# Optimization experiments

Measured on AMD Instinct MI355X. Metric: run time of the kernel, lower is better.

The kernel has to match this reference:

```python
import jax, jax.numpy as jnp
import numpy as np

NUM_CLASSES = 1024
TAU = 1.0


def setup_inputs() -> dict:
    key = jax.random.key(0)
    k1, k2, k3 = jax.random.split(key, 3)
    N_s, N_q, D = 65536, 65536, 512
    z_support = jax.random.normal(k1, (N_s, D), dtype=jnp.float32)
    y_support = jax.random.randint(k2, (N_s,), 0, NUM_CLASSES, dtype=jnp.int64)
    z_query = jax.random.normal(k3, (N_q, D), dtype=jnp.float32)
    return {"z_support": z_support, "y_support": y_support, "z_query": z_query}


def reference(z_support, y_support, z_query):
    # Per-class mean prototypes via a single segment reduce.
    # (Assumes all classes 0..C-1 appear in y_support, so torch.unique remap is identity.)
    sums = jax.ops.segment_sum(z_support, y_support, num_segments=NUM_CLASSES)  # [C, D]
    counts = jax.ops.segment_sum(
        jnp.ones((z_support.shape[0],), dtype=z_support.dtype),
        y_support, num_segments=NUM_CLASSES)  # [C]
    protos = sums / jnp.maximum(counts, 1.0)[:, None]  # [C, D]

    # Pairwise squared euclidean: ||q||^2 + ||p||^2 - 2 q.p
    q_sq = jnp.sum(z_query * z_query, axis=-1, keepdims=True)          # [Nq, 1]
    p_sq = jnp.sum(protos * protos, axis=-1)[None, :]                  # [1, C]
    cross = jnp.einsum("nd,cd->nc", z_query, protos)                   # [Nq, C]
    dist = q_sq + p_sq - 2.0 * cross
    logits = -TAU * dist
    return logits
```

## Files before the change

kernel.cpp:

```cpp
#include <hip/hip_runtime.h>
#include <stdint.h>

#define C_CLASSES 1024
#define D_DIM     512
#define N_SUP     65536
#define N_QRY     65536
#define SLOTS     144

typedef float f32x4 __attribute__((ext_vector_type(4)));
typedef float f32x16v __attribute__((ext_vector_type(16)));
typedef short bf16x8 __attribute__((ext_vector_type(8)));
typedef unsigned short u16x4 __attribute__((ext_vector_type(4)));
typedef unsigned short u16x8 __attribute__((ext_vector_type(8)));

#define GLOBAL_AS __attribute__((address_space(1)))
#define LDS_AS    __attribute__((address_space(3)))

__device__ inline void async_copy16(const void* g, void* l) {
    __builtin_amdgcn_global_load_lds((const GLOBAL_AS void*)g, (LDS_AS void*)l, 16, 0, 0);
}

__device__ inline unsigned short f2bf(float f) {
    union { float f; unsigned int u; } x; x.f = f;
    unsigned int u = x.u;
    return (unsigned short)((u + 0x7fffu + ((u >> 16) & 1u)) >> 16);
}

__global__ void init_kernel(int* __restrict__ cursors) {
    cursors[threadIdx.x] = 0;
}

template<bool CONV>
__global__ __launch_bounds__(256) void qsq_conv_kernel(
    const float* __restrict__ zq, float* __restrict__ qsq,
    unsigned short* __restrict__ Abf,
    const int* __restrict__ ys, int* __restrict__ cursors,
    int* __restrict__ rowlist)
{
    if (blockIdx.x < N_SUP / 256) {
        int i = blockIdx.x * 256 + threadIdx.x;
        int c = ys[i];
        int slot = atomicAdd(&cursors[c], 1);
        if (slot < SLOTS) rowlist[c * SLOTS + slot] = i;
    }

    const int w    = threadIdx.x >> 6;
    const int lane = threadIdx.x & 63;
    const int row  = blockIdx.x * 4 + w;
    const f32x4* zp = (const f32x4*)(zq + (size_t)row * D_DIM);
    f32x4 a = zp[2 * lane];
    f32x4 b = zp[2 * lane + 1];
    if (CONV) {
        u16x8 p;
        p.s0 = f2bf(a.x); p.s1 = f2bf(a.y); p.s2 = f2bf(a.z); p.s3 = f2bf(a.w);
        p.s4 = f2bf(b.x); p.s5 = f2bf(b.y); p.s6 = f2bf(b.z); p.s7 = f2bf(b.w);
        *(u16x8*)(Abf + (size_t)row * D_DIM + lane * 8) = p;
    }
    float s = a.x*a.x + a.y*a.y + a.z*a.z + a.w*a.w
            + b.x*b.x + b.y*b.y + b.z*b.z + b.w*b.w;
    #pragma unroll
    for (int off = 32; off > 0; off >>= 1) s += __shfl_down(s, off, 64);
    if (lane == 0) qsq[row] = s;
}

__global__ __launch_bounds__(256) void proto_gather(
    const float* __restrict__ zs, const int* __restrict__ rowlist,
    const int* __restrict__ cursors, unsigned short* __restrict__ protos,
    float* __restrict__ psq)
{
    const int c    = blockIdx.x;
    const int tid  = threadIdx.x;
    const int w    = tid >> 6;
    const int lane = tid & 63;

    const int cnt = cursors[c];
    const int m   = cnt < SLOTS ? cnt : SLOTS;

    __shared__ int sRows[SLOTS];
    if (tid < m) sRows[tid] = rowlist[c * SLOTS + tid];
    __syncthreads();

    f32x4 s0 = {0.f, 0.f, 0.f, 0.f};
    f32x4 s1 = {0.f, 0.f, 0.f, 0.f};
    int j = w;
    for (; j + 4 < m; j += 8) {
        int r0 = sRows[j];
        int r1 = sRows[j + 4];
        const f32x4* z0 = (const f32x4*)(zs + (size_t)r0 * D_DIM);
        const f32x4* z1 = (const f32x4*)(zs + (size_t)r1 * D_DIM);
        f32x4 a0 = z0[lane], a1 = z0[64 + lane];
        f32x4 b0 = z1[lane], b1 = z1[64 + lane];
        s0 += a0; s1 += a1;
        s0 += b0; s1 += b1;
    }
    for (; j < m; j += 4) {
        int r = sRows[j];
        const f32x4* zp = (const f32x4*)(zs + (size_t)r * D_DIM);
        s0 += zp[lane];
        s1 += zp[64 + lane];
    }

    __shared__ float sAcc[4][D_DIM];
    ((f32x4*)&sAcc[w][0])[lane]      = s0;
    ((f32x4*)&sAcc[w][0])[64 + lane] = s1;
    __syncthreads();

    float inv = 1.0f / fmaxf((float)cnt, 1.0f);
    int t2 = tid + 256;
    float p0 = (sAcc[0][tid] + sAcc[1][tid] + sAcc[2][tid] + sAcc[3][tid]) * inv;
    float p1 = (sAcc[0][t2]  + sAcc[1][t2]  + sAcc[2][t2]  + sAcc[3][t2])  * inv;
    protos[(size_t)c * D_DIM + tid] = f2bf(p0);
    protos[(size_t)c * D_DIM + t2]  = f2bf(p1);

    float ps = p0 * p0 + p1 * p1;
    #pragma unroll
    for (int off = 32; off > 0; off >>= 1) ps += __shfl_down(ps, off, 64);
    __shared__ float sPs[4];
    if (lane == 0) sPs[w] = ps;
    __syncthreads();
    if (tid == 0) psq[c] = sPs[0] + sPs[1] + sPs[2] + sPs[3];
}

template<bool FAST>
__global__ __launch_bounds__(256) void gemm_kernel(
    const float* __restrict__ A32, const unsigned short* __restrict__ Abf,
    const unsigned short* __restrict__ Bp,
    const float* __restrict__ qsq, const float* __restrict__ psq,
    float* __restrict__ out)
{
    constexpr int BM = 128, BN = 128, BK = 64, K = D_DIM, NN = C_CLASSES;
    __shared__ __align__(16) unsigned short shA[BM * BK];
    __shared__ __align__(16) unsigned short shB[BN * BK];

    const int tid  = threadIdx.x;
    const int lane = tid & 63;
    const int w    = tid >> 6;
    const int wm   = w >> 1, wn = w & 1;
    const int l31  = lane & 31, half = lane >> 5;
    const int mBase = blockIdx.y * BM;
    const int nBase = blockIdx.x * BN;

    const int srow = lane >> 3;
    const int scg  = ((lane & 7) ^ srow) * 8;

    f32x16v acc[2][2];
    #pragma unroll
    for (int i = 0; i < 2; i++)
        #pragma unroll
        for (int j = 0; j < 2; j++)
            acc[i][j] = (f32x16v)(0.0f);

    for (int k0 = 0; k0 < K; k0 += BK) {
        __syncthreads();
        if (FAST) {
            #pragma unroll
            for (int t = 0; t < 4; t++) {
                int g = w * 4 + t;
                async_copy16(Abf + (size_t)(mBase + g * 8 + srow) * K + k0 + scg,
                             &shA[g * 8 * BK]);
                async_copy16(Bp  + (size_t)(nBase + g * 8 + srow) * K + k0 + scg,
                             &shB[g * 8 * BK]);
            }
        } else {
            #pragma unroll
            for (int t = 0; t < 4; t++) {
                int q = tid * 4 + t;
                int r = q >> 3;
                int x = q & 7;
                int cg = x ^ (r & 7);
                const float* src = A32 + (size_t)(mBase + r) * K + k0 + cg * 8;
                f32x4 v0 = *(const f32x4*)src;
                f32x4 v1 = *(const f32x4*)(src + 4);
                u16x8 p;
                p.s0 = f2bf(v0.x); p.s1 = f2bf(v0.y); p.s2 = f2bf(v0.z); p.s3 = f2bf(v0.w);
                p.s4 = f2bf(v1.x); p.s5 = f2bf(v1.y); p.s6 = f2bf(v1.z); p.s7 = f2bf(v1.w);
                *(u16x8*)&shA[r * BK + x * 8] = p;
            }
            #pragma unroll
            for (int t = 0; t < 4; t++) {
                int g = w * 4 + t;
                async_copy16(Bp + (size_t)(nBase + g * 8 + srow) * K + k0 + scg,
                             &shB[g * 8 * BK]);
            }
        }
        __syncthreads();

        bf16x8 af[2][4], bfv[2][4];
        #pragma unroll
        for (int i = 0; i < 2; i++) {
            int ra = wm * 64 + i * 32 + l31;
            int ga = ra & 7;
            int rb = wn * 64 + i * 32 + l31;
            int gb = rb & 7;
            #pragma unroll
            for (int ks = 0; ks < 4; ks++) {
                int c = ks * 2 + half;
                af[i][ks]  = *(const bf16x8*)&shA[ra * BK + ((c ^ ga) * 8)];
                bfv[i][ks] = *(const bf16x8*)&shB[rb * BK + ((c ^ gb) * 8)];
            }
        }
        #pragma unroll
        for (int ks = 0; ks < 4; ks++)
            #pragma unroll
            for (int i = 0; i < 2; i++)
                #pragma unroll
                for (int j = 0; j < 2; j++)
                    acc[i][j] = __builtin_amdgcn_mfma_f32_32x32x16_bf16(
                        af[i][ks], bfv[j][ks], acc[i][j], 0, 0, 0);
    }

    const int rowb = mBase + wm * 64;
    const int colb = nBase + wn * 64;
    float pv[2];
    #pragma unroll
    for (int j = 0; j < 2; j++) pv[j] = psq[colb + j * 32 + l31];
    #pragma unroll
    for (int i = 0; i < 2; i++) {
        #pragma unroll
        for (int rg = 0; rg < 4; rg++) {
            int rbase = rowb + i * 32 + rg * 8 + half * 4;
            f32x4 qv = *(const f32x4*)&qsq[rbase];
            #pragma unroll
            for (int rr = 0; rr < 4; rr++) {
                int reg = rg * 4 + rr;
                size_t rowoff = (size_t)(rbase + rr) * NN;
                #pragma unroll
                for (int j = 0; j < 2; j++) {
                    out[rowoff + colb + j * 32 + l31] =
                        2.0f * acc[i][j][reg] - qv[rr] - pv[j];
                }
            }
        }
    }
}

extern "C" void kernel_launch(void* const* d_in, const int* in_sizes, int n_in,
                              void* d_out, int out_size, void* d_ws, size_t ws_size,
                              hipStream_t stream) {
    const float* zs = (const float*)d_in[0];
    const int*   ys = (const int*)d_in[1];
    const float* zq = (const float*)d_in[2];
    float* out = (float*)d_out;

    const size_t szAbf     = (size_t)N_QRY * D_DIM * 2;
    const size_t szProtos  = (size_t)C_CLASSES * D_DIM * 2;
    const size_t szQsq     = (size_t)N_QRY * 4;
    const size_t szRowlist = (size_t)C_CLASSES * SLOTS * 4;
    const size_t szPsq     = 4096;
    const size_t szCur     = 4096;

    const size_t needFast = szAbf + szProtos + szQsq + szRowlist + szPsq + szCur;
    const bool fast = ws_size >= needFast;

    char* ws = (char*)d_ws;
    unsigned short* Abf = (unsigned short*)ws;
    char* base = fast ? ws + szAbf : ws;
    unsigned short* protos = (unsigned short*)base;
    float* qsq  = (float*)(base + szProtos);
    int*   rowlist = (int*)(base + szProtos + szQsq);
    float* psq  = (float*)(base + szProtos + szQsq + szRowlist);
    int*   cursors = (int*)(base + szProtos + szQsq + szRowlist + szPsq);

    init_kernel<<<1, C_CLASSES, 0, stream>>>(cursors);
    if (fast)
        qsq_conv_kernel<true><<<N_QRY / 4, 256, 0, stream>>>(
            zq, qsq, Abf, ys, cursors, rowlist);
    else
        qsq_conv_kernel<false><<<N_QRY / 4, 256, 0, stream>>>(
            zq, qsq, nullptr, ys, cursors, rowlist);
    proto_gather<<<C_CLASSES, 256, 0, stream>>>(zs, rowlist, cursors, protos, psq);
    if (fast)
        gemm_kernel<true><<<dim3(C_CLASSES / 128, N_QRY / 128), 256, 0, stream>>>(
            nullptr, Abf, protos, qsq, psq, out);
    else
        gemm_kernel<false><<<dim3(C_CLASSES / 128, N_QRY / 128), 256, 0, stream>>>(
            zq, nullptr, protos, qsq, psq, out);
}
```

Before: 544.8 us.

## Use 256x256 double-buffered GEMM tiles with interleaved async staging

Replaces the fast-path 128x128 GEMM with a 256x256 tile kernel using 512 threads and double-buffered LDS. It issues async global-to-LDS loads for the next K slice while running MFMAs on the current one, and raises wave priority around the MFMA block. It also swaps the cursor-zeroing kernel for a memset. The larger tiles and double buffering use 128KB of LDS and more accumulator registers, which lowers occupancy and leaves fewer blocks to fill the grid.

```diff
diff --git a/kernel.cpp b/kernel.cpp
--- a/kernel.cpp
+++ b/kernel.cpp
@@ -24,10 +24,6 @@
     union { float f; unsigned int u; } x; x.f = f;
     unsigned int u = x.u;
     return (unsigned short)((u + 0x7fffu + ((u >> 16) & 1u)) >> 16);
-}
-
-__global__ void init_kernel(int* __restrict__ cursors) {
-    cursors[threadIdx.x] = 0;
 }
 
 template<bool CONV>
@@ -121,9 +117,142 @@
     if (tid == 0) psq[c] = sPs[0] + sPs[1] + sPs[2] + sPs[3];
 }
 
-template<bool FAST>
-__global__ __launch_bounds__(256) void gemm_kernel(
-    const float* __restrict__ A32, const unsigned short* __restrict__ Abf,
+__device__ __forceinline__ void stage_half(
+    const unsigned short* __restrict__ src,
+    unsigned short* dstTile,
+    int rowBase,
+    size_t gBase,
+    int k0, int srow, int scg)
+{
+    async_copy16(src + (gBase + (size_t)(rowBase + srow)) * D_DIM + k0 + scg,
+                 dstTile + (size_t)rowBase * 64);
+}
+
+__global__ __launch_bounds__(512, 2) void gemm256_kernel(
+    const unsigned short* __restrict__ Abf,
+    const unsigned short* __restrict__ Bp,
+    const float* __restrict__ qsq, const float* __restrict__ psq,
+    float* __restrict__ out)
+{
+    constexpr int BM = 256, BN = 256, BK = 64, K = D_DIM, NN = C_CLASSES;
+    constexpr int NKT = K / BK;
+    __shared__ __align__(16) unsigned short shA[2][BM * BK];
+    __shared__ __align__(16) unsigned short shB[2][BN * BK];
+
+    const int tid  = threadIdx.x;
+    const int lane = tid & 63;
+    const int w    = tid >> 6;
+    const int wm   = w >> 2, wn = w & 3;
+    const int l31  = lane & 31, half = lane >> 5;
+    const int mBase = blockIdx.y * BM;
+    const int nBase = blockIdx.x * BN;
+
+    const int srow = lane >> 3;
+    const int scg  = ((lane & 7) ^ srow) * 8;
+
+    f32x16v acc[4][2];
+    #pragma unroll
+    for (int i = 0; i < 4; i++)
+        #pragma unroll
+        for (int j = 0; j < 2; j++)
+            acc[i][j] = (f32x16v)(0.0f);
+
+    #pragma unroll
+    for (int t = 0; t < 2; t++) {
+        int rb = (w * 2 + t) * 8;
+        stage_half(Abf, &shA[0][0], rb,       mBase, 0, srow, scg);
+        stage_half(Abf, &shA[0][0], 128 + rb, mBase, 0, srow, scg);
+        stage_half(Bp,  &shB[0][0], rb,       nBase, 0, srow, scg);
+        stage_half(Bp,  &shB[0][0], 128 + rb, nBase, 0, srow, scg);
+    }
+    asm volatile("s_waitcnt vmcnt(0)" ::: "memory");
+    __builtin_amdgcn_s_barrier();
+
+    for (int kt = 0; kt < NKT; ++kt) {
+        const int kn = kt + 1;
+        unsigned short* curA = &shA[kt & 1][0];
+        unsigned short* curB = &shB[kt & 1][0];
+        unsigned short* nxtA = &shA[kn & 1][0];
+        unsigned short* nxtB = &shB[kn & 1][0];
+
+        bf16x8 bfv[2][4];
+
+        #pragma unroll
+        for (int p = 0; p < 4; ++p) {
+            bf16x8 af[4];
+            const int ra = wm * 128 + p * 32 + l31;
+            const int ga = ra & 7;
+            #pragma unroll
+            for (int ks = 0; ks < 4; ks++)
+                af[ks] = *(const bf16x8*)&curA[ra * BK + (((ks * 2 + half) ^ ga) * 8)];
+            if (p == 0) {
+                #pragma unroll
+                for (int n = 0; n < 2; n++) {
+                    const int rb = wn * 64 + n * 32 + l31;
+                    const int gb = rb & 7;
+                    #pragma unroll
+                    for (int ks = 0; ks < 4; ks++)
+                        bfv[n][ks] = *(const bf16x8*)&curB[rb * BK + (((ks * 2 + half) ^ gb) * 8)];
+                }
+            }
+
+            if (kn < NKT) {
+                const unsigned short* srcT = (p < 2) ? Abf : Bp;
+                unsigned short* dstT = (p < 2) ? nxtA : nxtB;
+                const size_t gb = (p < 2) ? (size_t)mBase : (size_t)nBase;
+                const int h = (p & 1) * 128;
+                #pragma unroll
+                for (int t = 0; t < 2; t++)
+                    stage_half(srcT, dstT, h + (w * 2 + t) * 8, gb, kn * BK, srow, scg);
+            }
+
+            asm volatile("" ::: "memory");
+            __builtin_amdgcn_s_barrier();
+
+            __builtin_amdgcn_s_setprio(1);
+            #pragma unroll
+            for (int ks = 0; ks < 4; ks++)
+                #pragma unroll
+                for (int n = 0; n < 2; n++)
+                    acc[p][n] = __builtin_amdgcn_mfma_f32_32x32x16_bf16(
+                        af[ks], bfv[n][ks], acc[p][n], 0, 0, 0);
+            __builtin_amdgcn_s_setprio(0);
+
+            if (p == 3)
+                asm volatile("s_waitcnt vmcnt(0) lgkmcnt(0)" ::: "memory");
+            else
+                asm volatile("s_waitcnt lgkmcnt(0)" ::: "memory");
+            __builtin_amdgcn_s_barrier();
+        }
+    }
+
+    const int rowb = mBase + wm * 128;
+    const int colb = nBase + wn * 64;
+    float pv[2];
+    #pragma unroll
+    for (int n = 0; n < 2; n++) pv[n] = psq[colb + n * 32 + l31];
+    #pragma unroll
+    for (int m = 0; m < 4; m++) {
+        #pragma unroll
+        for (int rg = 0; rg < 4; rg++) {
+            int rbase = rowb + m * 32 + rg * 8 + half * 4;
+            f32x4 qv = *(const f32x4*)&qsq[rbase];
+            #pragma unroll
+            for (int rr = 0; rr < 4; rr++) {
+                int reg = rg * 4 + rr;
+                size_t rowoff = (size_t)(rbase + rr) * NN;
+                #pragma unroll
+                for (int n = 0; n < 2; n++) {
+                    out[rowoff + colb + n * 32 + l31] =
+                        2.0f * acc[m][n][reg] - qv[rr] - pv[n];
+                }
+            }
+        }
+    }
+}
+
+__global__ __launch_bounds__(256) void gemm_kernel_slow(
+    const float* __restrict__ A32,
     const unsigned short* __restrict__ Bp,
     const float* __restrict__ qsq, const float* __restrict__ psq,
     float* __restrict__ out)
@@ -152,36 +281,25 @@
 
     for (int k0 = 0; k0 < K; k0 += BK) {
         __syncthreads();
-        if (FAST) {
-            #pragma unroll
-            for (int t = 0; t < 4; t++) {
-                int g = w * 4 + t;
-                async_copy16(Abf + (size_t)(mBase + g * 8 + srow) * K + k0 + scg,
-                             &shA[g * 8 * BK]);
-                async_copy16(Bp  + (size_t)(nBase + g * 8 + srow) * K + k0 + scg,
-                             &shB[g * 8 * BK]);
-            }
-        } else {
-            #pragma unroll
-            for (int t = 0; t < 4; t++) {
-                int q = tid * 4 + t;
-                int r = q >> 3;
-                int x = q & 7;
-                int cg = x ^ (r & 7);
-                const float* src = A32 + (size_t)(mBase + r) * K + k0 + cg * 8;
-                f32x4 v0 = *(const f32x4*)src;
-                f32x4 v1 = *(const f32x4*)(src + 4);
-                u16x8 p;
-                p.s0 = f2bf(v0.x); p.s1 = f2bf(v0.y); p.s2 = f2bf(v0.z); p.s3 = f2bf(v0.w);
-                p.s4 = f2bf(v1.x); p.s5 = f2bf(v1.y); p.s6 = f2bf(v1.z); p.s7 = f2bf(v1.w);
-                *(u16x8*)&shA[r * BK + x * 8] = p;
-            }
-            #pragma unroll
-            for (int t = 0; t < 4; t++) {
-                int g = w * 4 + t;
-                async_copy16(Bp + (size_t)(nBase + g * 8 + srow) * K + k0 + scg,
-                             &shB[g * 8 * BK]);
-            }
+        #pragma unroll
+        for (int t = 0; t < 4; t++) {
+            int q = tid * 4 + t;
+            int r = q >> 3;
+            int x = q & 7;
+            int cg = x ^ (r & 7);
+            const float* src = A32 + (size_t)(mBase + r) * K + k0 + cg * 8;
+            f32x4 v0 = *(const f32x4*)src;
+            f32x4 v1 = *(const f32x4*)(src + 4);
+            u16x8 p;
+            p.s0 = f2bf(v0.x); p.s1 = f2bf(v0.y); p.s2 = f2bf(v0.z); p.s3 = f2bf(v0.w);
+            p.s4 = f2bf(v1.x); p.s5 = f2bf(v1.y); p.s6 = f2bf(v1.z); p.s7 = f2bf(v1.w);
+            *(u16x8*)&shA[r * BK + x * 8] = p;
+        }
+        #pragma unroll
+        for (int t = 0; t < 4; t++) {
+            int g = w * 4 + t;
+            async_copy16(Bp + (size_t)(nBase + g * 8 + srow) * K + k0 + scg,
+                         &shB[g * 8 * BK]);
         }
         __syncthreads();
 
@@ -261,7 +379,8 @@
     float* psq  = (float*)(base + szProtos + szQsq + szRowlist);
     int*   cursors = (int*)(base + szProtos + szQsq + szRowlist + szPsq);
 
-    init_kernel<<<1, C_CLASSES, 0, stream>>>(cursors);
+    hipMemsetAsync(cursors, 0, C_CLASSES * sizeof(int), stream);
+
     if (fast)
         qsq_conv_kernel<true><<<N_QRY / 4, 256, 0, stream>>>(
             zq, qsq, Abf, ys, cursors, rowlist);
@@ -270,9 +389,9 @@
             zq, qsq, nullptr, ys, cursors, rowlist);
     proto_gather<<<C_CLASSES, 256, 0, stream>>>(zs, rowlist, cursors, protos, psq);
     if (fast)
-        gemm_kernel<true><<<dim3(C_CLASSES / 128, N_QRY / 128), 256, 0, stream>>>(
-            nullptr, Abf, protos, qsq, psq, out);
+        gemm256_kernel<<<dim3(C_CLASSES / 256, N_QRY / 256), 512, 0, stream>>>(
+            Abf, protos, qsq, psq, out);
     else
-        gemm_kernel<false><<<dim3(C_CLASSES / 128, N_QRY / 128), 256, 0, stream>>>(
-            zq, nullptr, protos, qsq, psq, out);
-}
+        gemm_kernel_slow<<<dim3(C_CLASSES / 128, N_QRY / 128), 256, 0, stream>>>(
+            zq, protos, qsq, psq, out);
+}
```

After: 541.1 us. About the same (-0.7%).
